# Kernel tuning notes

Hardware: AMD Instinct MI355X
Metric: run time of the kernel (lower is better)

Reference implementation:

```python
import jax, jax.numpy as jnp
import numpy as np

# ---- db4 filters (pywt conventions: dec_lo = rec_lo[::-1], rec_hi = qmf(rec_lo)) ----
F = 8  # db4 filter length
_rec_lo = np.array([0.23037781330885523, 0.7148465705525415, 0.6308807679295904,
                    -0.027983769416983849, -0.18703481171888114, 0.030841381835986965,
                    0.032883011666982945, -0.010597401784997278], dtype=np.float32)
_rec_hi = _rec_lo[::-1].copy()
_rec_hi[1::2] *= -1.0
REC_LO = jnp.asarray(_rec_lo)
REC_HI = jnp.asarray(_rec_hi)

MAX_LEVEL = 9  # pywt.dwt_max_level(4096, 8)


def _conv1d(x, kernel, stride=1, padding='VALID', lhs_dilation=None):
    # x: [B, L] -> correlation (XLA conv does NOT flip the kernel)
    out = jax.lax.conv_general_dilated(
        x[:, None, :], kernel[None, None, :],
        window_strides=(stride,), padding=padding,
        lhs_dilation=lhs_dilation,
        dimension_numbers=('NCH', 'OIH', 'NCH'))
    return out[:, 0, :]


def dwt(x):
    # pywt.dwt(x, 'db4', mode='symmetric'):
    # cA = np.convolve(sym_ext(x, F-1), dec_lo, 'valid')[1::2]
    # convolution with dec filter == correlation with rec filter (its reverse)
    ext = jnp.pad(x, ((0, 0), (F - 1, F - 1)), mode='symmetric')[:, 1:]
    return _conv1d(ext, REC_LO, stride=2), _conv1d(ext, REC_HI, stride=2)


def idwt(ca, cd):
    # pywt.idwt: zero-upsample coeffs, full convolution with rec filters, trim edges
    n = ca.shape[1]
    pad = ((F - 1, F - 1),)
    out = (_conv1d(ca, REC_LO[::-1], padding=pad, lhs_dilation=(2,)) +
           _conv1d(cd, REC_HI[::-1], padding=pad, lhs_dilation=(2,)))
    return out[:, F - 2:2 * n]  # output length = 2n - F + 2


def wavelet_features(x1):
    # Faithful to WaveletDWTLayer stack + WaveletParsingLayer: at each level k>=2,
    # reconstruct with details of levels k and k-1 only (others zeroed), with
    # pywt.waverec's trim-by-one rule; concatenate the 8 full-length reconstructions.
    a = x1
    cds, recs = [], []
    for level in range(1, MAX_LEVEL + 1):
        a, d = dwt(a)
        if level >= 2:
            r = idwt(jnp.zeros_like(d), d)
            for j in range(level - 2, -1, -1):
                dj = cds[j] if j == level - 2 else jnp.zeros_like(cds[j])
                if r.shape[1] == dj.shape[1] + 1:  # waverec trim rule
                    r = r[:, :-1]
                r = idwt(r, dj)
            recs.append(r)  # [B, signal_length]
        cds.append(d)
    return jnp.concatenate(recs, axis=1)  # [B, signal_length*(MAX_LEVEL-1)]


def reference(x1, x2, x3, W0, b0, W1, b1, W2, b2):
    # x2/x3 are placeholders in the original module (overwritten by layers 1/2)
    h = wavelet_features(x1)
    for W, b in ((W0, b0), (W1, b1), (W2, b2)):
        h = jax.nn.relu(h) @ W.T + b
    return h


def setup_inputs() -> dict:
    key = jax.random.key(0)
    ks = jax.random.split(key, 4)
    B, N = 2048, 4096
    D_IN, H1, H2, OUT = 32768, 181, 13, 10
    return {
        'x1': jax.random.normal(ks[0], (B, N), jnp.float32),
        'x2': jnp.zeros((B, 1, 8), jnp.float32),
        'x3': jnp.zeros((B, 1, 8), jnp.float32),
        'W0': jax.random.normal(ks[1], (H1, D_IN), jnp.float32) / np.float32(np.sqrt(D_IN)),
        'b0': jnp.zeros((H1,), jnp.float32),
        'W1': jax.random.normal(ks[2], (H2, H1), jnp.float32) / np.float32(np.sqrt(H1)),
        'b1': jnp.zeros((H2,), jnp.float32),
        'W2': jax.random.normal(ks[3], (OUT, H2), jnp.float32) / np.float32(np.sqrt(H2)),
        'b2': jnp.zeros((OUT,), jnp.float32),
    }
```

## Files before the change

### kernel.cpp

```cpp
#include <hip/hip_runtime.h>
#include <hip/hip_bf16.h>


typedef _Float16 f16x8 __attribute__((ext_vector_type(8)));
typedef _Float16 f16x4v __attribute__((ext_vector_type(4)));
typedef float f32x4 __attribute__((ext_vector_type(4)));

#define WV_THREADS 256
#define DROW 4160
#define NSPLIT 32
#define KCHUNK 1024

#define L0 0.23037781330885523f
#define L1 0.7148465705525415f
#define L2f 0.6308807679295904f
#define L3 -0.02798376941698385f
#define L4 -0.18703481171888114f
#define L5 0.030841381835986965f
#define L6 0.032883011666982945f
#define L7 -0.010597401784997278f

#define H0 -0.010597401784997278f
#define H1 -0.032883011666982945f
#define H2 0.030841381835986965f
#define H3 0.18703481171888114f
#define H4 -0.02798376941698385f
#define H5 -0.6308807679295904f
#define H6 0.7148465705525415f
#define H7 -0.23037781330885523f

__constant__ constexpr int cNL[10]   = {4096, 2051, 1029, 518, 262, 134, 70, 38, 22, 14};
__constant__ constexpr int cDOFF[10] = {0, 0, 2052, 3084, 3604, 3868, 4004, 4076, 4116, 4140};

__device__ __forceinline__ int ext_idx(int j, int n) {
  return (j < 6) ? (5 - j) : ((j < n + 6) ? (j - 6) : (2 * n + 5 - j));
}

__device__ __forceinline__ void dwt2(const float* a, float* anext, float* d,
                                     int n, int m, bool store_a) {
  const int ng = (m + 1) >> 1;
  for (int g = threadIdx.x; g < ng; g += WV_THREADS) {
    float w[10];
    if (g >= 2 && 4 * g + 9 <= n + 5) {
      const float2* af = (const float2*)a + (2 * g - 3);
      float2 b0 = af[0], b1 = af[1], b2 = af[2], b3 = af[3], b4 = af[4];
      w[0] = b0.x; w[1] = b0.y; w[2] = b1.x; w[3] = b1.y; w[4] = b2.x;
      w[5] = b2.y; w[6] = b3.x; w[7] = b3.y; w[8] = b4.x; w[9] = b4.y;
    } else {
#pragma unroll
      for (int q = 0; q < 10; ++q) {
        int j = 4 * g + q;
        int jm = n + 12;
        if (j > jm) j = jm;
        w[q] = a[ext_idx(j, n)];
      }
    }
    float sl0 = w[0]*L0 + w[1]*L1 + w[2]*L2f + w[3]*L3 + w[4]*L4 + w[5]*L5 + w[6]*L6 + w[7]*L7;
    float sh0 = w[0]*H0 + w[1]*H1 + w[2]*H2  + w[3]*H3 + w[4]*H4 + w[5]*H5 + w[6]*H6 + w[7]*H7;
    float sl1 = w[2]*L0 + w[3]*L1 + w[4]*L2f + w[5]*L3 + w[6]*L4 + w[7]*L5 + w[8]*L6 + w[9]*L7;
    float sh1 = w[2]*H0 + w[3]*H1 + w[4]*H2  + w[5]*H3 + w[6]*H4 + w[7]*H5 + w[8]*H6 + w[9]*H7;
    if (2 * g + 1 < m) {
      if (store_a) *(float2*)(anext + 2 * g) = make_float2(sl0, sl1);
      *(float2*)(d + 2 * g) = make_float2(sh0, sh1);
    } else {
      if (store_a) anext[2 * g] = sl0;
      d[2 * g] = sh0;
    }
  }
}

template <bool HAS_CA, bool HAS_CD, bool FINAL, int DLEN>
__device__ __forceinline__ void idwt4t(const float* ca, const float* cd,
                                       float* outl, _Float16* outg) {
  constexpr int npair = DLEN - 3;
  constexpr int ng4 = (npair + 3) >> 2;
#pragma unroll
  for (int t0 = 0; t0 < ng4; t0 += WV_THREADS) {
    const int t = t0 + (int)threadIdx.x;
    if (t < ng4) {
      float w[8], v[8];
      if (HAS_CA) {
        float4 A4 = ((const float4*)ca)[t];
        float4 B4 = ((const float4*)ca)[t + 1];
        w[0]=A4.x; w[1]=A4.y; w[2]=A4.z; w[3]=A4.w;
        w[4]=B4.x; w[5]=B4.y; w[6]=B4.z; w[7]=B4.w;
      }
      if (HAS_CD) {
        float4 C4 = ((const float4*)cd)[t];
        float4 D4 = ((const float4*)cd)[t + 1];
        v[0]=C4.x; v[1]=C4.y; v[2]=C4.z; v[3]=C4.w;
        v[4]=D4.x; v[5]=D4.y; v[6]=D4.z; v[7]=D4.w;
      }
      float e[4], o[4];
#pragma unroll
      for (int q = 0; q < 4; ++q) {
        float eq = 0.f, oq = 0.f;
        if (HAS_CA) {
          eq = w[q+3]*L0 + w[q+2]*L2f + w[q+1]*L4 + w[q]*L6;
          oq = w[q+3]*L1 + w[q+2]*L3  + w[q+1]*L5 + w[q]*L7;
        }
        if (HAS_CD) {
          eq += v[q+3]*H0 + v[q+2]*H2 + v[q+1]*H4 + v[q]*H6;
          oq += v[q+3]*H1 + v[q+2]*H3 + v[q+1]*H5 + v[q]*H7;
        }
        e[q] = eq; o[q] = oq;
      }
      if (FINAL) {
        f16x8 h;
        h[0] = (_Float16)fmaxf(e[0], 0.f); h[1] = (_Float16)fmaxf(o[0], 0.f);
        h[2] = (_Float16)fmaxf(e[1], 0.f); h[3] = (_Float16)fmaxf(o[1], 0.f);
        h[4] = (_Float16)fmaxf(e[2], 0.f); h[5] = (_Float16)fmaxf(o[2], 0.f);
        h[6] = (_Float16)fmaxf(e[3], 0.f); h[7] = (_Float16)fmaxf(o[3], 0.f);
        *(f16x8*)(outg + 8 * t) = h;
      } else {
        if (4 * t + 3 < npair) {
          ((float4*)(outl + 8 * t))[0] = make_float4(e[0], o[0], e[1], o[1]);
          ((float4*)(outl + 8 * t))[1] = make_float4(e[2], o[2], e[3], o[3]);
        } else {
#pragma unroll
          for (int q = 0; q < 4; ++q)
            if (4 * t + q < npair)
              *(float2*)(outl + 8 * t + 2 * q) = make_float2(e[q], o[q]);
        }
      }
    }
  }
}

template <int L>
__device__ __forceinline__ void synth_cascade(const float* dr, _Float16* og,
                                              float* s1, float* s2) {
  idwt4t<false, true, false, cNL[L]>(nullptr, dr + cDOFF[L], s1, nullptr);
  __syncthreads();
  float* cur = s1;
  float* nxt = s2;
  if constexpr (L >= 3) {
    idwt4t<true, true, false, cNL[L - 1]>(cur, dr + cDOFF[L - 1], nxt, nullptr);
    __syncthreads();
    float* t = cur; cur = nxt; nxt = t;
  }
#define NOCD_STEP(DL)                                             \
  {                                                               \
    idwt4t<true, false, false, DL>(cur, nullptr, nxt, nullptr);   \
    __syncthreads();                                              \
    float* t = cur; cur = nxt; nxt = t;                           \
  }
  if constexpr (L >= 9) NOCD_STEP(cNL[7])
  if constexpr (L >= 8) NOCD_STEP(cNL[6])
  if constexpr (L >= 7) NOCD_STEP(cNL[5])
  if constexpr (L >= 6) NOCD_STEP(cNL[4])
  if constexpr (L >= 5) NOCD_STEP(cNL[3])
  if constexpr (L >= 4) NOCD_STEP(cNL[2])
#undef NOCD_STEP
  idwt4t<true, (L == 2), true, 2051>(cur, (L == 2) ? dr + cDOFF[1] : nullptr,
                                     nullptr, og);
}

__global__ __launch_bounds__(WV_THREADS) void wv_analysis_cvt(
    const float* __restrict__ x, float* __restrict__ dG,
    const float* __restrict__ W0, _Float16* __restrict__ Bw) {
  __shared__ float r1[4104];
  __shared__ float r2[2056];
  const int tid = threadIdx.x;

  if (blockIdx.x >= 2048) {
    size_t i = ((size_t)(blockIdx.x - 2048) * 256 + tid) * 4;
    int rowc = (int)(i >> 15);
    f16x4v h;
    if (rowc < 181) {
      const float4 v = *(const float4*)(W0 + i);
      h[0] = (_Float16)v.x; h[1] = (_Float16)v.y;
      h[2] = (_Float16)v.z; h[3] = (_Float16)v.w;
    } else {
      h[0] = (_Float16)0.f; h[1] = (_Float16)0.f;
      h[2] = (_Float16)0.f; h[3] = (_Float16)0.f;
    }
    *(f16x4v*)(Bw + i) = h;
    return;
  }

  const int NLa[10]  = {4096, 2051, 1029, 518, 262, 134, 70, 38, 22, 14};
  const int DOFF[10] = {0, 0, 2052, 3084, 3604, 3868, 4004, 4076, 4116, 4140};
  const int LOFF[10] = {0, 0, 1036, 520, 2068, 1040, 2332, 1176, 2404, 1216};
  const int row = blockIdx.x;

  const float4* xr = (const float4*)(x + (size_t)row * 4096);
  for (int i = tid; i < 1024; i += WV_THREADS) ((float4*)r1)[i] = xr[i];
  __syncthreads();

  float* dr = dG + (size_t)row * DROW;
  dwt2(r1, r2, dr + DOFF[1], NLa[0], NLa[1], true);
  __syncthreads();
  const float* ap = r2;
  float* an = r1;
  for (int lev = 2; lev <= 9; ++lev) {
    float* dbuf = ((lev & 1) ? r2 : r1) + LOFF[lev];
    dwt2(ap, an, dbuf, NLa[lev - 1], NLa[lev], lev < 9);
    __syncthreads();
    const float* t = ap; ap = an; an = (float*)t;
  }
  for (int lev = 2; lev <= 9; ++lev) {
    const float* src = ((lev & 1) ? r2 : r1) + LOFF[lev];
    float* dst = dr + DOFF[lev];
    const int n = NLa[lev];
    for (int i = 2 * tid; i + 1 < n; i += 2 * WV_THREADS)
      *(float2*)(dst + i) = *(const float2*)(src + i);
    if ((n & 1) && tid == 0) dst[n - 1] = src[n - 1];
  }
}

__global__ __launch_bounds__(WV_THREADS, 6) void wv_synth(
    const float* __restrict__ dG, _Float16* __restrict__ A) {
  __shared__ float s1[2052];
  __shared__ float s2[2052];
  const int row = blockIdx.x;
  const float* dr = dG + (size_t)row * DROW;
  _Float16* og = A + (size_t)row * 32768 + (size_t)blockIdx.y * 4096;
  switch (blockIdx.y) {
    case 0: synth_cascade<2>(dr, og, s1, s2); break;
    case 1: synth_cascade<3>(dr, og, s1, s2); break;
    case 2: synth_cascade<4>(dr, og, s1, s2); break;
    case 3: synth_cascade<5>(dr, og, s1, s2); break;
    case 4: synth_cascade<6>(dr, og, s1, s2); break;
    case 5: synth_cascade<7>(dr, og, s1, s2); break;
    case 6: synth_cascade<8>(dr, og, s1, s2); break;
    default: synth_cascade<9>(dr, og, s1, s2); break;
  }
}

__device__ __forceinline__ void load_lds16(const void* g, void* l) {
  __builtin_amdgcn_global_load_lds((__attribute__((address_space(1))) unsigned int*)g,
                                   (__attribute__((address_space(3))) unsigned int*)l,
                                   16, 0, 0);
}

__global__ __launch_bounds__(256, 2) void gemm_kernel(
    const _Float16* __restrict__ A, const _Float16* __restrict__ Bw,
    float* __restrict__ P) {
  __shared__ _Float16 As[128 * 64];
  __shared__ _Float16 Bs[192 * 64];
  const int tid = threadIdx.x;
  const int lane = tid & 63;
  const int wave = tid >> 6;
  const int m0 = blockIdx.x * 128;
  const int k_idx = blockIdx.y;
  const int k0 = k_idx * KCHUNK;

  f32x4 acc[2][12];
#pragma unroll
  for (int mt = 0; mt < 2; ++mt)
#pragma unroll
    for (int nt = 0; nt < 12; ++nt) acc[mt][nt] = (f32x4){0.f, 0.f, 0.f, 0.f};

  for (int ks = 0; ks < (KCHUNK >> 6); ++ks) {
    const int kbase = k0 + (ks << 6);
    __syncthreads();
#pragma unroll
    for (int t = 0; t < 4; ++t) {
      int g = ((wave * 4 + t) << 6) + lane;
      int r = g >> 3, cs = g & 7;
      const _Float16* gp = A + (size_t)(m0 + r) * 32768 + kbase + ((cs ^ (r & 7)) << 3);
      load_lds16(gp, (char*)As + (size_t)((wave * 4 + t) << 10));
    }
#pragma unroll
    for (int t = 0; t < 6; ++t) {
      int g = ((wave * 6 + t) << 6) + lane;
      int r = g >> 3, cs = g & 7;
      const _Float16* gp = Bw + (size_t)r * 32768 + kbase + ((cs ^ (r & 7)) << 3);
      load_lds16(gp, (char*)Bs + (size_t)((wave * 6 + t) << 10));
    }
    __syncthreads();
#pragma unroll
    for (int kk = 0; kk < 2; ++kk) {
      const int chunk = kk * 4 + (lane >> 4);
      f16x8 af[2];
#pragma unroll
      for (int mt = 0; mt < 2; ++mt) {
        int r = wave * 32 + mt * 16 + (lane & 15);
        af[mt] = *(const f16x8*)(As + r * 64 + ((chunk ^ (r & 7)) << 3));
      }
#pragma unroll
      for (int nt = 0; nt < 12; ++nt) {
        int rb = nt * 16 + (lane & 15);
        f16x8 bf = *(const f16x8*)(Bs + rb * 64 + ((chunk ^ (rb & 7)) << 3));
        acc[0][nt] = __builtin_amdgcn_mfma_f32_16x16x32_f16(af[0], bf, acc[0][nt], 0, 0, 0);
        acc[1][nt] = __builtin_amdgcn_mfma_f32_16x16x32_f16(af[1], bf, acc[1][nt], 0, 0, 0);
      }
    }
  }
  float* Pp = P + ((size_t)k_idx * 2048 + m0) * 192;
#pragma unroll
  for (int mt = 0; mt < 2; ++mt)
#pragma unroll
    for (int nt = 0; nt < 12; ++nt)
#pragma unroll
      for (int r4 = 0; r4 < 4; ++r4) {
        int rr = wave * 32 + mt * 16 + ((lane >> 4) << 2) + r4;
        int cc = nt * 16 + (lane & 15);
        Pp[(size_t)rr * 192 + cc] = acc[mt][nt][r4];
      }
}

__global__ __launch_bounds__(256) void mlp_kernel(
    const float* __restrict__ P, const float* __restrict__ b0,
    const float* __restrict__ W1, const float* __restrict__ b1,
    const float* __restrict__ W2, const float* __restrict__ b2,
    float* __restrict__ out) {
  __shared__ float part[4][193];
  __shared__ float h1[192];
  __shared__ float h2[13];
  const int row = blockIdx.x;
  const int t = threadIdx.x;
  const int g = t >> 6;
  const int l = t & 63;

  float a0 = 0.f, a1 = 0.f, a2 = 0.f;
  for (int si = 0; si < NSPLIT / 4; ++si) {
    int s = g + (si << 2);
    const float* Pr = P + ((size_t)s * 2048 + row) * 192;
    a0 += Pr[l]; a1 += Pr[64 + l]; a2 += Pr[128 + l];
  }
  part[g][l] = a0; part[g][64 + l] = a1; part[g][128 + l] = a2;
  __syncthreads();

  if (t < 192) {
    float v = part[0][t] + part[1][t] + part[2][t] + part[3][t];
    h1[t] = (t < 181) ? fmaxf(v + b0[t], 0.f) : 0.f;
  }
  __syncthreads();

#pragma unroll
  for (int r = 0; r < 4; ++r) {
    int j = g + (r << 2);
    if (j < 13) {
      float v = 0.f;
#pragma unroll
      for (int q = 0; q < 3; ++q) {
        int n = l + (q << 6);
        if (n < 181) v += h1[n] * W1[j * 181 + n];
      }
      for (int off = 32; off >= 1; off >>= 1) v += __shfl_down(v, off);
      if (l == 0) h2[j] = fmaxf(v + b1[j], 0.f);
    }
  }
  __syncthreads();

  if (t < 10) {
    float c = b2[t];
#pragma unroll
    for (int j = 0; j < 13; ++j) c += h2[j] * W2[t * 13 + j];
    out[(size_t)row * 10 + t] = c;
  }
}

extern "C" void kernel_launch(void* const* d_in, const int* in_sizes, int n_in,
                              void* d_out, int out_size, void* d_ws, size_t ws_size,
                              hipStream_t stream) {
  const float* x1 = (const float*)d_in[0];
  const float* W0 = (const float*)d_in[3];
  const float* b0 = (const float*)d_in[4];
  const float* W1 = (const float*)d_in[5];
  const float* b1 = (const float*)d_in[6];
  const float* W2 = (const float*)d_in[7];
  const float* b2 = (const float*)d_in[8];
  float* out = (float*)d_out;

  char* ws = (char*)d_ws;
  const size_t A_BYTES = (size_t)2048 * 32768 * 2;
  const size_t B_BYTES = (size_t)192 * 32768 * 2;
  _Float16* Afeat = (_Float16*)ws;
  _Float16* Bw = (_Float16*)(ws + A_BYTES);
  float* Dq = (float*)(ws + A_BYTES + B_BYTES);
  float* P = (float*)(ws + A_BYTES + B_BYTES);

  wv_analysis_cvt<<<2048 + 6144, WV_THREADS, 0, stream>>>(x1, Dq, W0, Bw);
  dim3 sg(2048, 8);
  wv_synth<<<sg, WV_THREADS, 0, stream>>>(Dq, Afeat);
  dim3 gg(16, NSPLIT);
  gemm_kernel<<<gg, 256, 0, stream>>>(Afeat, Bw, P);
  mlp_kernel<<<2048, 256, 0, stream>>>(P, b0, W1, b1, W2, b2, out);
}
```

Measured before the change: 218.6 us.

## Fuse pairs of inverse-DWT synthesis levels in registers with swizzled LDS

The synthesis cascade now runs two consecutive approximation-only inverse-DWT levels per pass in registers (pair16/finpair16), with 16 outputs per thread. This halves the number of LDS round trips and __syncthreads barriers per row. The first two levels (detail L and L-1) are also fused into one initpair16 step that reads both detail bands straight from global memory. LDS accesses use an XOR swizzle to cut bank conflicts, and occupancy is raised to 8 blocks per SM. The cost is more register pressure and some redundant halo computation, and the swizzle indexing and level-length bookkeeping are easy to get wrong.

```diff
diff --git a/kernel.cpp b/kernel.cpp
--- a/kernel.cpp
+++ b/kernel.cpp
@@ -69,91 +69,216 @@
   }
 }
 
-template <bool HAS_CA, bool HAS_CD, bool FINAL, int DLEN>
-__device__ __forceinline__ void idwt4t(const float* ca, const float* cd,
+#define SWZ(u) ((u) ^ (((u) >> 3) & 7))
+__device__ __forceinline__ const float4* lds4c(const float* b, int s) {
+  return (const float4*)b + SWZ(s);
+}
+__device__ __forceinline__ float4* lds4(float* b, int s) {
+  return (float4*)b + SWZ(s);
+}
+
+template <bool HAS_CA, bool HAS_CD, bool FINAL, int N>
+__device__ __forceinline__ void step16(const float* ca, const float* cd,
                                        float* outl, _Float16* outg) {
-  constexpr int npair = DLEN - 3;
-  constexpr int ng4 = (npair + 3) >> 2;
-#pragma unroll
-  for (int t0 = 0; t0 < ng4; t0 += WV_THREADS) {
-    const int t = t0 + (int)threadIdx.x;
-    if (t < ng4) {
-      float w[8], v[8];
-      if (HAS_CA) {
-        float4 A4 = ((const float4*)ca)[t];
-        float4 B4 = ((const float4*)ca)[t + 1];
-        w[0]=A4.x; w[1]=A4.y; w[2]=A4.z; w[3]=A4.w;
-        w[4]=B4.x; w[5]=B4.y; w[6]=B4.z; w[7]=B4.w;
+  constexpr int npair = N - 3;
+  constexpr int ng = (npair + 7) >> 3;
+  const int t = threadIdx.x;
+  if (t >= ng) return;
+  float w[12], v[12];
+  if constexpr (HAS_CA) {
+    float4 a = *lds4c(ca, 2 * t), b = *lds4c(ca, 2 * t + 1), c = *lds4c(ca, 2 * t + 2);
+    w[0]=a.x; w[1]=a.y; w[2]=a.z; w[3]=a.w; w[4]=b.x; w[5]=b.y; w[6]=b.z; w[7]=b.w;
+    w[8]=c.x; w[9]=c.y; w[10]=c.z; w[11]=c.w;
+  }
+  if constexpr (HAS_CD) {
+    const float4* p = (const float4*)(cd + 8 * t);
+    float4 a = p[0], b = p[1], c = p[2];
+    v[0]=a.x; v[1]=a.y; v[2]=a.z; v[3]=a.w; v[4]=b.x; v[5]=b.y; v[6]=b.z; v[7]=b.w;
+    v[8]=c.x; v[9]=c.y; v[10]=c.z; v[11]=c.w;
+  }
+  float E[8], O[8];
+#pragma unroll
+  for (int pp = 0; pp < 8; ++pp) {
+    float e = 0.f, o = 0.f;
+    if constexpr (HAS_CA) {
+      e = w[pp+3]*L0 + w[pp+2]*L2f + w[pp+1]*L4 + w[pp]*L6;
+      o = w[pp+3]*L1 + w[pp+2]*L3  + w[pp+1]*L5 + w[pp]*L7;
+    }
+    if constexpr (HAS_CD) {
+      e += v[pp+3]*H0 + v[pp+2]*H2 + v[pp+1]*H4 + v[pp]*H6;
+      o += v[pp+3]*H1 + v[pp+2]*H3 + v[pp+1]*H5 + v[pp]*H7;
+    }
+    E[pp] = e; O[pp] = o;
+  }
+  if constexpr (FINAL) {
+    f16x8 h0, h1;
+    h0[0]=(_Float16)fmaxf(E[0],0.f); h0[1]=(_Float16)fmaxf(O[0],0.f);
+    h0[2]=(_Float16)fmaxf(E[1],0.f); h0[3]=(_Float16)fmaxf(O[1],0.f);
+    h0[4]=(_Float16)fmaxf(E[2],0.f); h0[5]=(_Float16)fmaxf(O[2],0.f);
+    h0[6]=(_Float16)fmaxf(E[3],0.f); h0[7]=(_Float16)fmaxf(O[3],0.f);
+    h1[0]=(_Float16)fmaxf(E[4],0.f); h1[1]=(_Float16)fmaxf(O[4],0.f);
+    h1[2]=(_Float16)fmaxf(E[5],0.f); h1[3]=(_Float16)fmaxf(O[5],0.f);
+    h1[4]=(_Float16)fmaxf(E[6],0.f); h1[5]=(_Float16)fmaxf(O[6],0.f);
+    h1[6]=(_Float16)fmaxf(E[7],0.f); h1[7]=(_Float16)fmaxf(O[7],0.f);
+    *(f16x8*)(outg + 16 * t) = h0;
+    *(f16x8*)(outg + 16 * t + 8) = h1;
+  } else {
+#pragma unroll
+    for (int j = 0; j < 4; ++j) {
+      const int p2 = 8 * t + 2 * j;
+      if (p2 + 1 < npair) {
+        *lds4(outl, 4 * t + j) = make_float4(E[2*j], O[2*j], E[2*j+1], O[2*j+1]);
+      } else if (p2 < npair) {
+        *(float2*)lds4(outl, 4 * t + j) = make_float2(E[2*j], O[2*j]);
       }
-      if (HAS_CD) {
-        float4 C4 = ((const float4*)cd)[t];
-        float4 D4 = ((const float4*)cd)[t + 1];
-        v[0]=C4.x; v[1]=C4.y; v[2]=C4.z; v[3]=C4.w;
-        v[4]=D4.x; v[5]=D4.y; v[6]=D4.z; v[7]=D4.w;
-      }
-      float e[4], o[4];
-#pragma unroll
-      for (int q = 0; q < 4; ++q) {
-        float eq = 0.f, oq = 0.f;
-        if (HAS_CA) {
-          eq = w[q+3]*L0 + w[q+2]*L2f + w[q+1]*L4 + w[q]*L6;
-          oq = w[q+3]*L1 + w[q+2]*L3  + w[q+1]*L5 + w[q]*L7;
-        }
-        if (HAS_CD) {
-          eq += v[q+3]*H0 + v[q+2]*H2 + v[q+1]*H4 + v[q]*H6;
-          oq += v[q+3]*H1 + v[q+2]*H3 + v[q+1]*H5 + v[q]*H7;
-        }
-        e[q] = eq; o[q] = oq;
-      }
-      if (FINAL) {
-        f16x8 h;
-        h[0] = (_Float16)fmaxf(e[0], 0.f); h[1] = (_Float16)fmaxf(o[0], 0.f);
-        h[2] = (_Float16)fmaxf(e[1], 0.f); h[3] = (_Float16)fmaxf(o[1], 0.f);
-        h[4] = (_Float16)fmaxf(e[2], 0.f); h[5] = (_Float16)fmaxf(o[2], 0.f);
-        h[6] = (_Float16)fmaxf(e[3], 0.f); h[7] = (_Float16)fmaxf(o[3], 0.f);
-        *(f16x8*)(outg + 8 * t) = h;
-      } else {
-        if (4 * t + 3 < npair) {
-          ((float4*)(outl + 8 * t))[0] = make_float4(e[0], o[0], e[1], o[1]);
-          ((float4*)(outl + 8 * t))[1] = make_float4(e[2], o[2], e[3], o[3]);
-        } else {
-#pragma unroll
-          for (int q = 0; q < 4; ++q)
-            if (4 * t + q < npair)
-              *(float2*)(outl + 8 * t + 2 * q) = make_float2(e[q], o[q]);
-        }
-      }
+    }
+  }
+}
+
+__device__ __forceinline__ void nocd2_core(const float w[12], float r[11],
+                                           float E[8], float O[8]) {
+#pragma unroll
+  for (int h = 0; h < 6; ++h) {
+    float e = w[h+3]*L0 + w[h+2]*L2f + w[h+1]*L4 + w[h]*L6;
+    float o = w[h+3]*L1 + w[h+2]*L3  + w[h+1]*L5 + w[h]*L7;
+    r[2*h] = e;
+    if (2*h + 1 < 11) r[2*h+1] = o;
+  }
+#pragma unroll
+  for (int pp = 0; pp < 8; ++pp) {
+    E[pp] = r[pp+3]*L0 + r[pp+2]*L2f + r[pp+1]*L4 + r[pp]*L6;
+    O[pp] = r[pp+3]*L1 + r[pp+2]*L3  + r[pp+1]*L5 + r[pp]*L7;
+  }
+}
+
+template <int N1>
+__device__ __forceinline__ void pair16(const float* cur, float* outl) {
+  constexpr int N2 = (2 * N1 - 6 == 1030) ? 1029 : (2 * N1 - 6);
+  constexpr int np2 = N2 - 3;
+  constexpr int ng = (np2 + 7) >> 3;
+  const int t = threadIdx.x;
+  if (t >= ng) return;
+  float w[12];
+  float4 a = *lds4c(cur, t), b = *lds4c(cur, t + 1), c = *lds4c(cur, t + 2);
+  w[0]=a.x; w[1]=a.y; w[2]=a.z; w[3]=a.w; w[4]=b.x; w[5]=b.y; w[6]=b.z; w[7]=b.w;
+  w[8]=c.x; w[9]=c.y; w[10]=c.z; w[11]=c.w;
+  float r[11], E[8], O[8];
+  nocd2_core(w, r, E, O);
+#pragma unroll
+  for (int j = 0; j < 4; ++j) {
+    const int p2 = 8 * t + 2 * j;
+    if (p2 + 1 < np2) {
+      *lds4(outl, 4 * t + j) = make_float4(E[2*j], O[2*j], E[2*j+1], O[2*j+1]);
+    } else if (p2 < np2) {
+      *(float2*)lds4(outl, 4 * t + j) = make_float2(E[2*j], O[2*j]);
+    }
+  }
+}
+
+__device__ __forceinline__ void finpair16(const float* cur, _Float16* outg) {
+  const int t = threadIdx.x;
+  float w[12];
+  float4 a = *lds4c(cur, t), b = *lds4c(cur, t + 1), c = *lds4c(cur, t + 2);
+  w[0]=a.x; w[1]=a.y; w[2]=a.z; w[3]=a.w; w[4]=b.x; w[5]=b.y; w[6]=b.z; w[7]=b.w;
+  w[8]=c.x; w[9]=c.y; w[10]=c.z; w[11]=c.w;
+  float r[11], E[8], O[8];
+  nocd2_core(w, r, E, O);
+  f16x8 h0, h1;
+  h0[0]=(_Float16)fmaxf(E[0],0.f); h0[1]=(_Float16)fmaxf(O[0],0.f);
+  h0[2]=(_Float16)fmaxf(E[1],0.f); h0[3]=(_Float16)fmaxf(O[1],0.f);
+  h0[4]=(_Float16)fmaxf(E[2],0.f); h0[5]=(_Float16)fmaxf(O[2],0.f);
+  h0[6]=(_Float16)fmaxf(E[3],0.f); h0[7]=(_Float16)fmaxf(O[3],0.f);
+  h1[0]=(_Float16)fmaxf(E[4],0.f); h1[1]=(_Float16)fmaxf(O[4],0.f);
+  h1[2]=(_Float16)fmaxf(E[5],0.f); h1[3]=(_Float16)fmaxf(O[5],0.f);
+  h1[4]=(_Float16)fmaxf(E[6],0.f); h1[5]=(_Float16)fmaxf(O[6],0.f);
+  h1[6]=(_Float16)fmaxf(E[7],0.f); h1[7]=(_Float16)fmaxf(O[7],0.f);
+  *(f16x8*)(outg + 16 * t) = h0;
+  *(f16x8*)(outg + 16 * t + 8) = h1;
+}
+
+template <int NL, int NLm1>
+__device__ __forceinline__ void initpair16(const float* cdL, const float* cdm,
+                                           float* outl) {
+  constexpr int np2 = NLm1 - 3;
+  constexpr int ng = (np2 + 7) >> 3;
+  const int t = threadIdx.x;
+  if (t >= ng) return;
+  float w[12];
+  {
+    const float4* p = (const float4*)(cdL + 4 * t);
+    float4 a = p[0], b = p[1], c = p[2];
+    w[0]=a.x; w[1]=a.y; w[2]=a.z; w[3]=a.w; w[4]=b.x; w[5]=b.y; w[6]=b.z; w[7]=b.w;
+    w[8]=c.x; w[9]=c.y; w[10]=c.z; w[11]=c.w;
+  }
+  float r[11];
+#pragma unroll
+  for (int h = 0; h < 6; ++h) {
+    float e = w[h+3]*H0 + w[h+2]*H2 + w[h+1]*H4 + w[h]*H6;
+    float o = w[h+3]*H1 + w[h+2]*H3 + w[h+1]*H5 + w[h]*H7;
+    r[2*h] = e;
+    if (2*h + 1 < 11) r[2*h+1] = o;
+  }
+  float v[12];
+  {
+    const float4* p = (const float4*)(cdm + 8 * t);
+    float4 a = p[0], b = p[1], c = p[2];
+    v[0]=a.x; v[1]=a.y; v[2]=a.z; v[3]=a.w; v[4]=b.x; v[5]=b.y; v[6]=b.z; v[7]=b.w;
+    v[8]=c.x; v[9]=c.y; v[10]=c.z; v[11]=c.w;
+  }
+  float E[8], O[8];
+#pragma unroll
+  for (int pp = 0; pp < 8; ++pp) {
+    E[pp] = r[pp+3]*L0 + r[pp+2]*L2f + r[pp+1]*L4 + r[pp]*L6
+          + v[pp+3]*H0 + v[pp+2]*H2  + v[pp+1]*H4 + v[pp]*H6;
+    O[pp] = r[pp+3]*L1 + r[pp+2]*L3  + r[pp+1]*L5 + r[pp]*L7
+          + v[pp+3]*H1 + v[pp+2]*H3  + v[pp+1]*H5 + v[pp]*H7;
+  }
+#pragma unroll
+  for (int j = 0; j < 4; ++j) {
+    const int p2 = 8 * t + 2 * j;
+    if (p2 + 1 < np2) {
+      *lds4(outl, 4 * t + j) = make_float4(E[2*j], O[2*j], E[2*j+1], O[2*j+1]);
+    } else if (p2 < np2) {
+      *(float2*)lds4(outl, 4 * t + j) = make_float2(E[2*j], O[2*j]);
     }
   }
 }
 
 template <int L>
-__device__ __forceinline__ void synth_cascade(const float* dr, _Float16* og,
-                                              float* s1, float* s2) {
-  idwt4t<false, true, false, cNL[L]>(nullptr, dr + cDOFF[L], s1, nullptr);
-  __syncthreads();
-  float* cur = s1;
-  float* nxt = s2;
-  if constexpr (L >= 3) {
-    idwt4t<true, true, false, cNL[L - 1]>(cur, dr + cDOFF[L - 1], nxt, nullptr);
+__device__ __forceinline__ void synth2(const float* dr, _Float16* og,
+                                       float* s1, float* s2) {
+  if constexpr (L == 2) {
+    step16<false, true, false, 1029>(nullptr, dr + cDOFF[2], s1, nullptr);
     __syncthreads();
-    float* t = cur; cur = nxt; nxt = t;
-  }
-#define NOCD_STEP(DL)                                             \
-  {                                                               \
-    idwt4t<true, false, false, DL>(cur, nullptr, nxt, nullptr);   \
-    __syncthreads();                                              \
-    float* t = cur; cur = nxt; nxt = t;                           \
-  }
-  if constexpr (L >= 9) NOCD_STEP(cNL[7])
-  if constexpr (L >= 8) NOCD_STEP(cNL[6])
-  if constexpr (L >= 7) NOCD_STEP(cNL[5])
-  if constexpr (L >= 6) NOCD_STEP(cNL[4])
-  if constexpr (L >= 5) NOCD_STEP(cNL[3])
-  if constexpr (L >= 4) NOCD_STEP(cNL[2])
-#undef NOCD_STEP
-  idwt4t<true, (L == 2), true, 2051>(cur, (L == 2) ? dr + cDOFF[1] : nullptr,
-                                     nullptr, og);
+    step16<true, true, true, 2051>(s1, dr + cDOFF[1], nullptr, og);
+  } else {
+    initpair16<cNL[L], cNL[L - 1]>(dr + cDOFF[L], dr + cDOFF[L - 1], s1);
+    __syncthreads();
+    if constexpr (L == 3) {
+      step16<true, false, true, 2051>(s1, nullptr, nullptr, og);
+    } else if constexpr (L == 4) {
+      finpair16(s1, og);
+    } else if constexpr (L == 5) {
+      pair16<518>(s1, s2); __syncthreads();
+      step16<true, false, true, 2051>(s2, nullptr, nullptr, og);
+    } else if constexpr (L == 6) {
+      pair16<262>(s1, s2); __syncthreads();
+      finpair16(s2, og);
+    } else if constexpr (L == 7) {
+      pair16<134>(s1, s2); __syncthreads();
+      pair16<518>(s2, s1); __syncthreads();
+      step16<true, false, true, 2051>(s1, nullptr, nullptr, og);
+    } else if constexpr (L == 8) {
+      pair16<70>(s1, s2); __syncthreads();
+      pair16<262>(s2, s1); __syncthreads();
+      finpair16(s1, og);
+    } else {
+      pair16<38>(s1, s2); __syncthreads();
+      pair16<134>(s1 ? s2 : s2, s1); __syncthreads();
+      pair16<518>(s1, s2); __syncthreads();
+      step16<true, false, true, 2051>(s2, nullptr, nullptr, og);
+    }
+  }
 }
 
 __global__ __launch_bounds__(WV_THREADS) void wv_analysis_cvt(
@@ -209,22 +334,22 @@
   }
 }
 
-__global__ __launch_bounds__(WV_THREADS, 6) void wv_synth(
+__global__ __launch_bounds__(WV_THREADS, 8) void wv_synth(
     const float* __restrict__ dG, _Float16* __restrict__ A) {
-  __shared__ float s1[2052];
-  __shared__ float s2[2052];
+  __shared__ alignas(16) float s1[2080];
+  __shared__ alignas(16) float s2[2080];
   const int row = blockIdx.x;
   const float* dr = dG + (size_t)row * DROW;
   _Float16* og = A + (size_t)row * 32768 + (size_t)blockIdx.y * 4096;
   switch (blockIdx.y) {
-    case 0: synth_cascade<2>(dr, og, s1, s2); break;
-    case 1: synth_cascade<3>(dr, og, s1, s2); break;
-    case 2: synth_cascade<4>(dr, og, s1, s2); break;
-    case 3: synth_cascade<5>(dr, og, s1, s2); break;
-    case 4: synth_cascade<6>(dr, og, s1, s2); break;
-    case 5: synth_cascade<7>(dr, og, s1, s2); break;
-    case 6: synth_cascade<8>(dr, og, s1, s2); break;
-    default: synth_cascade<9>(dr, og, s1, s2); break;
+    case 0: synth2<2>(dr, og, s1, s2); break;
+    case 1: synth2<3>(dr, og, s1, s2); break;
+    case 2: synth2<4>(dr, og, s1, s2); break;
+    case 3: synth2<5>(dr, og, s1, s2); break;
+    case 4: synth2<6>(dr, og, s1, s2); break;
+    case 5: synth2<7>(dr, og, s1, s2); break;
+    case 6: synth2<8>(dr, og, s1, s2); break;
+    default: synth2<9>(dr, og, s1, s2); break;
   }
 }
 
```

Measured after the change: 223.0 us. 2.0% more time.
